# Kernel tuning notes

Hardware: AMD Instinct MI355X
Metric: run time of the kernel (lower is better)

## Reference

```python
import jax, jax.numpy as jnp
import numpy as np
from jax import lax

CHUNK = 64          # rows per chunk in the parabola pass (bounds peak memory)
INF = jnp.float32(1e12)  # 'no site in this column' sentinel for squared distance


def _edt_sq(mask):
    """Exact squared Euclidean distance transform of a 2D bool mask.

    Matches scipy.ndimage.distance_transform_edt(mask)**2: for pixels where
    mask is True (nonzero), squared distance to the nearest False (zero)
    pixel; 0 at False pixels. Separable: 1D along-column distance, then a
    brute-force lower-envelope (parabola) pass along rows, which is exact.
    """
    h, w = mask.shape
    sites = ~mask  # zero pixels = distance sources
    idx = jnp.arange(h, dtype=jnp.int32)[:, None]  # [H,1]
    # distance (in rows) to nearest site above / below in the same column
    up = idx - lax.cummax(jnp.where(sites, idx, -h), axis=0)
    down = lax.cummin(jnp.where(sites, idx, 2 * h), axis=0, reverse=True) - idx
    d = jnp.minimum(up, down)  # >= h means no site in this column
    g = jnp.where(d >= h, INF, d.astype(jnp.float32) ** 2)  # [H,W]

    # parabola pass along axis 1: out[r, j] = min_k g[r, k] + (j-k)^2
    j = jnp.arange(w, dtype=jnp.float32)
    dk2 = (j[:, None] - j[None, :]) ** 2  # [W_j, W_k]

    def row_chunk(gc):  # gc: [CHUNK, W]
        return jnp.min(gc[:, None, :] + dk2[None, :, :], axis=-1)

    gch = g.reshape(h // CHUNK, CHUNK, w)
    return lax.map(row_chunk, gch).reshape(h, w)


def _signed_distance(t):
    """t: bool foreground mask. Returns inside*(~t) - (outside-1)*t, where
    outside = EDT(t) (fg pixel -> nearest bg) and inside = EDT(~t)
    (bg pixel -> nearest fg), as in the original distance_metric."""
    outside = jnp.sqrt(_edt_sq(t))
    inside = jnp.sqrt(_edt_sq(~t))
    tf = t.astype(jnp.float32)
    return inside * (1.0 - tf) - (outside - 1.0) * tf


def setup_inputs() -> dict:
    key = jax.random.key(0)
    k1, k2 = jax.random.split(key)
    inp = jax.random.normal(k1, (1024, 1024), dtype=jnp.float32)
    target = jax.random.randint(k2, (1024, 1024), 0, 2, dtype=jnp.int32)
    return {"input": inp, "target": target}


def reference(input, target):
    sd = _signed_distance(target != 0)
    return jnp.mean(input * sd)
```

## Files before the change

kernel.cpp:

```cpp
#include <hip/hip_runtime.h>

#define H 1024
#define W 1024
#define NPIX (H * W)
#define WW 16
#define INF_F 1e12f
#define THREADS 256
#define BIG (1 << 29)

__device__ __noinline__ int vert_dist_full(const unsigned long long* __restrict__ pw,
                                           int r, int c, int pol) {
  int w = r >> 6, b = r & 63;
  unsigned long long v = pw[w * W + c];
  unsigned long long m_c = pol ? v : ~v;
  int dup = 1 << 30, ddn = 1 << 30;
  unsigned long long am = m_c & ((1ULL << b) - 1ULL);
  if (am) {
    dup = b - (63 - __builtin_clzll(am));
  } else {
    for (int ww = w - 1; ww >= 0; --ww) {
      unsigned long long mv = pw[ww * W + c];
      mv = pol ? mv : ~mv;
      if (mv) { dup = r - (ww * 64 + 63 - __builtin_clzll(mv)); break; }
    }
  }
  unsigned long long bm = m_c >> b;
  if (bm) {
    ddn = __builtin_ctzll(bm);
  } else {
    for (int ww = w + 1; ww < WW; ++ww) {
      unsigned long long mv = pw[ww * W + c];
      mv = pol ? mv : ~mv;
      if (mv) { ddn = (ww * 64 + __builtin_ctzll(mv)) - r; break; }
    }
  }
  return min(dup, ddn);
}

__device__ __noinline__ int horiz_exact(const unsigned long long* __restrict__ pw,
                                        int r, int c, int pol, int best, int dk0) {
  for (int dk = dk0; dk < W; ++dk) {
    int dk2 = dk * dk;
    if (dk2 >= best) break;
    if (c - dk >= 0) {
      int d = vert_dist_full(pw, r, c - dk, pol);
      if (d < H) best = min(best, d * d + dk2);
    }
    if (c + dk < W) {
      int d = vert_dist_full(pw, r, c + dk, pol);
      if (d < H) best = min(best, d * d + dk2);
    }
  }
  return best;
}

__global__ __launch_bounds__(THREADS) void pack_bits(
    const int* __restrict__ target, unsigned short* __restrict__ pw16) {
  int tg = blockIdx.x * THREADS + threadIdx.x;
  int c = tg & (W - 1);
  int rest = tg >> 10;
  int w = rest >> 2;
  int quarter = rest & 3;
  int rbase = w * 64 + quarter * 16;
  unsigned int val = 0;
#pragma unroll
  for (int b = 0; b < 16; ++b) {
    if (target[(rbase + b) * W + c] != 0) val |= (1u << b);
  }
  pw16[((w * W + c) << 2) + quarter] = (unsigned short)val;
}

__global__ __launch_bounds__(THREADS) void fused_edt_row(
    const unsigned long long* __restrict__ pw,
    const float* __restrict__ input,
    double* __restrict__ partials) {
  __shared__ unsigned char sd8[2][W + 64];
  const int tid = threadIdx.x;
  const int r = blockIdx.x;
  const int w = r >> 6, b = r & 63;
  const int c0 = tid << 2;

  const float4 iv = *(const float4*)(input + r * W + c0);

  if (tid < 32) {
    int p = tid >> 4, q = tid & 15;
    ((unsigned int*)sd8)[p * 272 + (q < 8 ? q : 256 + q)] = 0xFFFFFFFFu;
  }

  unsigned long long curv[4], prevv[4], nextv[4];
  *(ulonglong2*)&curv[0] = *(const ulonglong2*)(pw + w * W + c0);
  *(ulonglong2*)&curv[2] = *(const ulonglong2*)(pw + w * W + c0 + 2);
  const bool hp = (w > 0), hn = (w < WW - 1);
  if (hp) {
    *(ulonglong2*)&prevv[0] = *(const ulonglong2*)(pw + (w - 1) * W + c0);
    *(ulonglong2*)&prevv[2] = *(const ulonglong2*)(pw + (w - 1) * W + c0 + 2);
  } else prevv[0] = prevv[1] = prevv[2] = prevv[3] = 0ULL;
  if (hn) {
    *(ulonglong2*)&nextv[0] = *(const ulonglong2*)(pw + (w + 1) * W + c0);
    *(ulonglong2*)&nextv[2] = *(const ulonglong2*)(pw + (w + 1) * W + c0 + 2);
  } else nextv[0] = nextv[1] = nextv[2] = nextv[3] = 0ULL;

  unsigned char dloc[2][4];
#pragma unroll
  for (int pol = 0; pol < 2; ++pol) {
#pragma unroll
    for (int k = 0; k < 4; ++k) {
      unsigned long long m_c = pol ? curv[k] : ~curv[k];
      unsigned long long m_p = hp ? (pol ? prevv[k] : ~prevv[k]) : 0ULL;
      unsigned long long m_n = hn ? (pol ? nextv[k] : ~nextv[k]) : 0ULL;
      int d = 1 << 30;
      unsigned long long am = m_c & ((1ULL << b) - 1ULL);
      if (am) d = b - (63 - __builtin_clzll(am));
      else if (m_p) d = b + 1 + __builtin_clzll(m_p);
      unsigned long long bm = m_c >> b;
      int dd = 1 << 30;
      if (bm) dd = __builtin_ctzll(bm);
      else if (m_n) dd = (64 - b) + __builtin_ctzll(m_n);
      d = min(d, dd);
      if (d > 64) d = vert_dist_full(pw, r, c0 + k, pol);
      dloc[pol][k] = (unsigned char)min(d, 255);
    }
  }
#pragma unroll
  for (int pol = 0; pol < 2; ++pol) {
    unsigned int u = (unsigned int)dloc[pol][0] |
                     ((unsigned int)dloc[pol][1] << 8) |
                     ((unsigned int)dloc[pol][2] << 16) |
                     ((unsigned int)dloc[pol][3] << 24);
    *(unsigned int*)&sd8[pol][32 + c0] = u;
  }
  __syncthreads();

  double val = 0.0;
  const float ivk[4] = {iv.x, iv.y, iv.z, iv.w};
#pragma unroll
  for (int k = 0; k < 4; ++k) {
    const bool t = (dloc[1][k] == 0);
    const int pol = t ? 0 : 1;
    const int own = dloc[pol][k];
    int best = (own == 255) ? BIG : own * own;
    const unsigned char* __restrict__ sg = &sd8[pol][32 + c0 + k];
#pragma unroll
    for (int dk = 1; dk <= 2; ++dk) {
      int dl = sg[-dk], dr = sg[dk];
      int gl = (dl == 255) ? BIG : dl * dl;
      int gr = (dr == 255) ? BIG : dr * dr;
      best = min(best, min(gl, gr) + dk * dk);
    }
    for (int dk = 3; dk <= 32; ++dk) {
      int dk2 = dk * dk;
      if (dk2 >= best) break;
      int dl = sg[-dk], dr = sg[dk];
      int gl = (dl == 255) ? BIG : dl * dl;
      int gr = (dr == 255) ? BIG : dr * dr;
      best = min(best, min(gl, gr) + dk2);
    }
    if (best > 1089) {
      int c = c0 + k;
      if (best > 65025) {
        int ov = vert_dist_full(pw, r, c, pol);
        best = (ov < H) ? ov * ov : (1 << 30);
        best = horiz_exact(pw, r, c, pol, best, 1);
      } else {
        best = horiz_exact(pw, r, c, pol, best, 33);
      }
    }
    float bestf = (best >= BIG) ? INF_F : (float)best;
    float dist = sqrtf(bestf);
    float sd = t ? (1.0f - dist) : dist;
    val += (double)(ivk[k] * sd);
  }

  for (int off = 32; off > 0; off >>= 1)
    val += __shfl_down(val, off, 64);
  __shared__ double smem[THREADS / 64];
  int lane = tid & 63, wid = tid >> 6;
  if (lane == 0) smem[wid] = val;
  __syncthreads();
  if (tid == 0)
    partials[blockIdx.x] = smem[0] + smem[1] + smem[2] + smem[3];
}

__global__ __launch_bounds__(THREADS) void reduce_partials(
    const double* __restrict__ partials, float* __restrict__ out) {
  double s = 0.0;
#pragma unroll
  for (int i = 0; i < 4; ++i) s += partials[threadIdx.x + i * THREADS];
  for (int off = 32; off > 0; off >>= 1)
    s += __shfl_down(s, off, 64);
  __shared__ double smem[THREADS / 64];
  int lane = threadIdx.x & 63, wid = threadIdx.x >> 6;
  if (lane == 0) smem[wid] = s;
  __syncthreads();
  if (threadIdx.x == 0)
    out[0] = (float)((smem[0] + smem[1] + smem[2] + smem[3]) / (double)NPIX);
}

extern "C" void kernel_launch(void* const* d_in, const int* in_sizes, int n_in,
                              void* d_out, int out_size, void* d_ws, size_t ws_size,
                              hipStream_t stream) {
  const float* input = (const float*)d_in[0];
  const int* target = (const int*)d_in[1];
  float* out = (float*)d_out;

  double* partials = (double*)d_ws;
  unsigned long long* pw = (unsigned long long*)((char*)d_ws + 8192);

  pack_bits<<<256, THREADS, 0, stream>>>(target, (unsigned short*)pw);
  fused_edt_row<<<H, THREADS, 0, stream>>>(pw, input, partials);
  reduce_partials<<<1, THREADS, 0, stream>>>(partials, out);
}
```

Measured before the change: 65.66 us.

## Split each row across two blocks with 32-column halos, two pixels per thread

Each image row is now handled by two blocks covering 512 columns each, and every thread processes two pixels instead of four. The vertical distances for 32 halo columns on each side are computed by the first 64 threads so the local parabola search stays exact within the window. Launch bounds now request higher occupancy, and the partials buffer and reduction grow to 2048 entries. The aim is more parallelism and shorter per-thread critical paths, at the cost of redundant halo work and an extra load pass for halo columns.

```diff
diff --git a/kernel.cpp b/kernel.cpp
--- a/kernel.cpp
+++ b/kernel.cpp
@@ -6,6 +6,8 @@
 #define WW 16
 #define INF_F 1e12f
 #define THREADS 256
+#define CB 512
+#define RBLOCKS (2 * H)
 #define BIG (1 << 29)
 
 __device__ __noinline__ int vert_dist_full(const unsigned long long* __restrict__ pw,
@@ -70,76 +72,85 @@
   pw16[((w * W + c) << 2) + quarter] = (unsigned short)val;
 }
 
-__global__ __launch_bounds__(THREADS) void fused_edt_row(
+__global__ __launch_bounds__(THREADS, 8) void fused_edt_row(
     const unsigned long long* __restrict__ pw,
     const float* __restrict__ input,
     double* __restrict__ partials) {
-  __shared__ unsigned char sd8[2][W + 64];
+  __shared__ unsigned char sd8[2][CB + 64];
+  __shared__ double smem[THREADS / 64];
   const int tid = threadIdx.x;
-  const int r = blockIdx.x;
+  const int bid = blockIdx.x;
+  const int r = bid >> 1;
+  const int cb = (bid & 1) << 9;
   const int w = r >> 6, b = r & 63;
-  const int c0 = tid << 2;
-
-  const float4 iv = *(const float4*)(input + r * W + c0);
-
-  if (tid < 32) {
-    int p = tid >> 4, q = tid & 15;
-    ((unsigned int*)sd8)[p * 272 + (q < 8 ? q : 256 + q)] = 0xFFFFFFFFu;
-  }
-
-  unsigned long long curv[4], prevv[4], nextv[4];
-  *(ulonglong2*)&curv[0] = *(const ulonglong2*)(pw + w * W + c0);
-  *(ulonglong2*)&curv[2] = *(const ulonglong2*)(pw + w * W + c0 + 2);
+  const int c0 = cb + (tid << 1);
+
+  const float2 iv = *(const float2*)(input + r * W + c0);
+
   const bool hp = (w > 0), hn = (w < WW - 1);
-  if (hp) {
-    *(ulonglong2*)&prevv[0] = *(const ulonglong2*)(pw + (w - 1) * W + c0);
-    *(ulonglong2*)&prevv[2] = *(const ulonglong2*)(pw + (w - 1) * W + c0 + 2);
-  } else prevv[0] = prevv[1] = prevv[2] = prevv[3] = 0ULL;
-  if (hn) {
-    *(ulonglong2*)&nextv[0] = *(const ulonglong2*)(pw + (w + 1) * W + c0);
-    *(ulonglong2*)&nextv[2] = *(const ulonglong2*)(pw + (w + 1) * W + c0 + 2);
-  } else nextv[0] = nextv[1] = nextv[2] = nextv[3] = 0ULL;
-
-  unsigned char dloc[2][4];
+
+  unsigned long long curv[2], prevv[2], nextv[2];
+  *(ulonglong2*)curv = *(const ulonglong2*)(pw + w * W + c0);
+  if (hp) *(ulonglong2*)prevv = *(const ulonglong2*)(pw + (w - 1) * W + c0);
+  else prevv[0] = prevv[1] = 0ULL;
+  if (hn) *(ulonglong2*)nextv = *(const ulonglong2*)(pw + (w + 1) * W + c0);
+  else nextv[0] = nextv[1] = 0ULL;
+
+  const int hcol = (tid < 32) ? (cb - 32 + tid) : (cb + CB + (tid - 32));
+  const bool hvalid = (tid < 64) && (hcol >= 0) && (hcol < W);
+  unsigned long long hcur = 0ULL, hprev = 0ULL, hnext = 0ULL;
+  if (hvalid) {
+    hcur = pw[w * W + hcol];
+    if (hp) hprev = pw[(w - 1) * W + hcol];
+    if (hn) hnext = pw[(w + 1) * W + hcol];
+  }
+
+  auto vdist = [&](unsigned long long cv, unsigned long long pv,
+                   unsigned long long nv, int pol, int c) -> unsigned char {
+    unsigned long long m_c = pol ? cv : ~cv;
+    unsigned long long m_p = hp ? (pol ? pv : ~pv) : 0ULL;
+    unsigned long long m_n = hn ? (pol ? nv : ~nv) : 0ULL;
+    int d = 1 << 30;
+    unsigned long long am = m_c & ((1ULL << b) - 1ULL);
+    if (am) d = b - (63 - __builtin_clzll(am));
+    else if (m_p) d = b + 1 + __builtin_clzll(m_p);
+    unsigned long long bm = m_c >> b;
+    int dd = 1 << 30;
+    if (bm) dd = __builtin_ctzll(bm);
+    else if (m_n) dd = (64 - b) + __builtin_ctzll(m_n);
+    d = min(d, dd);
+    if (d > 64) d = vert_dist_full(pw, r, c, pol);
+    return (unsigned char)min(d, 255);
+  };
+
+  unsigned char dloc[2][2];
 #pragma unroll
   for (int pol = 0; pol < 2; ++pol) {
 #pragma unroll
-    for (int k = 0; k < 4; ++k) {
-      unsigned long long m_c = pol ? curv[k] : ~curv[k];
-      unsigned long long m_p = hp ? (pol ? prevv[k] : ~prevv[k]) : 0ULL;
-      unsigned long long m_n = hn ? (pol ? nextv[k] : ~nextv[k]) : 0ULL;
-      int d = 1 << 30;
-      unsigned long long am = m_c & ((1ULL << b) - 1ULL);
-      if (am) d = b - (63 - __builtin_clzll(am));
-      else if (m_p) d = b + 1 + __builtin_clzll(m_p);
-      unsigned long long bm = m_c >> b;
-      int dd = 1 << 30;
-      if (bm) dd = __builtin_ctzll(bm);
-      else if (m_n) dd = (64 - b) + __builtin_ctzll(m_n);
-      d = min(d, dd);
-      if (d > 64) d = vert_dist_full(pw, r, c0 + k, pol);
-      dloc[pol][k] = (unsigned char)min(d, 255);
-    }
-  }
-#pragma unroll
-  for (int pol = 0; pol < 2; ++pol) {
-    unsigned int u = (unsigned int)dloc[pol][0] |
-                     ((unsigned int)dloc[pol][1] << 8) |
-                     ((unsigned int)dloc[pol][2] << 16) |
-                     ((unsigned int)dloc[pol][3] << 24);
-    *(unsigned int*)&sd8[pol][32 + c0] = u;
+    for (int k = 0; k < 2; ++k)
+      dloc[pol][k] = vdist(curv[k], prevv[k], nextv[k], pol, c0 + k);
+    *(unsigned short*)&sd8[pol][32 + (tid << 1)] =
+        (unsigned short)((unsigned int)dloc[pol][0] |
+                         ((unsigned int)dloc[pol][1] << 8));
+  }
+  if (tid < 64) {
+    int idx = (tid < 32) ? tid : (CB + tid);
+#pragma unroll
+    for (int pol = 0; pol < 2; ++pol)
+      sd8[pol][idx] = hvalid ? vdist(hcur, hprev, hnext, pol, hcol)
+                             : (unsigned char)255;
   }
   __syncthreads();
 
   double val = 0.0;
-  const float ivk[4] = {iv.x, iv.y, iv.z, iv.w};
-#pragma unroll
-  for (int k = 0; k < 4; ++k) {
+  const float ivk[2] = {iv.x, iv.y};
+#pragma unroll
+  for (int k = 0; k < 2; ++k) {
     const bool t = (dloc[1][k] == 0);
     const int pol = t ? 0 : 1;
     const int own = dloc[pol][k];
     int best = (own == 255) ? BIG : own * own;
-    const unsigned char* __restrict__ sg = &sd8[pol][32 + c0 + k];
+    const unsigned char* __restrict__ sg = &sd8[pol][32 + (tid << 1) + k];
 #pragma unroll
     for (int dk = 1; dk <= 2; ++dk) {
       int dl = sg[-dk], dr = sg[dk];
@@ -173,19 +184,18 @@
 
   for (int off = 32; off > 0; off >>= 1)
     val += __shfl_down(val, off, 64);
-  __shared__ double smem[THREADS / 64];
   int lane = tid & 63, wid = tid >> 6;
   if (lane == 0) smem[wid] = val;
   __syncthreads();
   if (tid == 0)
-    partials[blockIdx.x] = smem[0] + smem[1] + smem[2] + smem[3];
+    partials[bid] = smem[0] + smem[1] + smem[2] + smem[3];
 }
 
 __global__ __launch_bounds__(THREADS) void reduce_partials(
     const double* __restrict__ partials, float* __restrict__ out) {
   double s = 0.0;
 #pragma unroll
-  for (int i = 0; i < 4; ++i) s += partials[threadIdx.x + i * THREADS];
+  for (int i = 0; i < 8; ++i) s += partials[threadIdx.x + i * THREADS];
   for (int off = 32; off > 0; off >>= 1)
     s += __shfl_down(s, off, 64);
   __shared__ double smem[THREADS / 64];
@@ -204,9 +214,9 @@
   float* out = (float*)d_out;
 
   double* partials = (double*)d_ws;
-  unsigned long long* pw = (unsigned long long*)((char*)d_ws + 8192);
+  unsigned long long* pw = (unsigned long long*)((char*)d_ws + 32768);
 
   pack_bits<<<256, THREADS, 0, stream>>>(target, (unsigned short*)pw);
-  fused_edt_row<<<H, THREADS, 0, stream>>>(pw, input, partials);
+  fused_edt_row<<<RBLOCKS, THREADS, 0, stream>>>(pw, input, partials);
   reduce_partials<<<1, THREADS, 0, stream>>>(partials, out);
 }
```

After: 66.38 us. No clear change (+1.1%).
